# Performance work log

Measured on AMD Instinct MI355X. Metric: run time of the kernel, lower is better.

## Reference

```python
import jax, jax.numpy as jnp
import numpy as np

B, T, C = 1, 2048, 2048
H, KH, HD = 16, 4, 128  # n_head, n_kv_head, head_dim
ROPE_BASE = 10000.0


def setup_inputs() -> dict:
    key = jax.random.key(0)
    ks = jax.random.split(key, 5)
    s = 0.02
    return {
        "x": jax.random.normal(ks[0], (B, T, C), jnp.float32),
        "Wq": jax.random.normal(ks[1], (C, H * HD), jnp.float32) * s,
        "Wk": jax.random.normal(ks[2], (C, KH * HD), jnp.float32) * s,
        "Wv": jax.random.normal(ks[3], (C, KH * HD), jnp.float32) * s,
        "Wo": jax.random.normal(ks[4], (H * HD, C), jnp.float32) * s,
        "position_ids": jnp.arange(T, dtype=jnp.int32),
    }


def _rotate_half(a):
    h = a.shape[-1] // 2
    return jnp.concatenate([-a[..., h:], a[..., :h]], axis=-1)


def reference(x, Wq, Wk, Wv, Wo, position_ids):
    b, t, c = x.shape
    n_rep = H // KH
    # projections -> [B, heads, T, HD]
    q = (x @ Wq).reshape(b, t, H, HD).transpose(0, 2, 1, 3)
    k = (x @ Wk).reshape(b, t, KH, HD).transpose(0, 2, 1, 3)
    v = (x @ Wv).reshape(b, t, KH, HD).transpose(0, 2, 1, 3)
    # rotary embedding cache [T, HD]
    inv_freq = 1.0 / (ROPE_BASE ** (jnp.arange(0, HD, 2, dtype=jnp.float32) / HD))
    pos = jnp.arange(t, dtype=jnp.float32)
    freqs = pos[:, None] * inv_freq[None, :]
    emb = jnp.concatenate([freqs, freqs], axis=-1)
    cos = jnp.cos(emb)[position_ids][None, None]  # [1,1,T,HD]
    sin = jnp.sin(emb)[position_ids][None, None]
    q = q * cos + _rotate_half(q) * sin
    k = k * cos + _rotate_half(k) * sin
    # GQA: group query heads instead of materializing repeated K/V
    qg = q.reshape(b, KH, n_rep, t, HD)
    scale = jnp.float32(1.0 / np.sqrt(HD))
    scores = jnp.einsum('bgrtd,bgsd->bgrts', qg, k) * scale
    causal = jnp.tril(jnp.ones((t, t), dtype=bool))
    scores = jnp.where(causal, scores, jnp.float32(-1e30))
    p = jax.nn.softmax(scores, axis=-1)
    y = jnp.einsum('bgrts,bgsd->bgrtd', p, v)
    y = y.reshape(b, H, t, HD).transpose(0, 2, 1, 3).reshape(b, t, H * HD)
    return y @ Wo
```

## Files before the change

kernel.cpp:

```cpp
#include <hip/hip_runtime.h>

typedef unsigned short u16;
using bf16x8 = __attribute__((ext_vector_type(8))) short;
using f32x4  = __attribute__((ext_vector_type(4))) float;

#define GLD16(g, l)                                                            \
  __builtin_amdgcn_global_load_lds(                                            \
      (const __attribute__((address_space(1))) void*)(g),                      \
      (__attribute__((address_space(3))) void*)(l), 16, 0, 0)

__device__ __forceinline__ u16 f2b(float x) {
  union { float f; unsigned u; } v; v.f = x;
  unsigned r = v.u + 0x7FFF + ((v.u >> 16) & 1);
  return (u16)(r >> 16);
}

__global__ void cast_bf16_kernel(const float* __restrict__ in,
                                 u16* __restrict__ out, int n4) {
  int i = blockIdx.x * blockDim.x + threadIdx.x;
  int stride = gridDim.x * blockDim.x;
  for (; i < n4; i += stride) {
    float4 v = ((const float4*)in)[i];
    ushort4 o;
    o.x = f2b(v.x); o.y = f2b(v.y); o.z = f2b(v.z); o.w = f2b(v.w);
    ((ushort4*)out)[i] = o;
  }
}

__global__ void transpose_w_kernel(const float* __restrict__ src,
                                   u16* __restrict__ dst, int K, int N) {
  __shared__ float tile[32][33];
  int n0 = blockIdx.x * 32, k0 = blockIdx.y * 32;
  int tx = threadIdx.x, ty = threadIdx.y;
#pragma unroll
  for (int r = 0; r < 4; r++)
    tile[ty + r * 8][tx] = src[(size_t)(k0 + ty + r * 8) * N + n0 + tx];
  __syncthreads();
#pragma unroll
  for (int r = 0; r < 4; r++)
    dst[(size_t)(n0 + ty + r * 8) * K + k0 + tx] = f2b(tile[tx][ty + r * 8]);
}

__global__ void transpose_v_kernel(const u16* __restrict__ src,
                                   u16* __restrict__ dst) {
  __shared__ u16 tile[32][33];
  int h = blockIdx.z;
  int t0 = blockIdx.x * 32, d0 = blockIdx.y * 32;
  const u16* s = src + (size_t)h * 2048 * 128;
  u16* d = dst + (size_t)h * 128 * 2048;
  int tx = threadIdx.x, ty = threadIdx.y;
#pragma unroll
  for (int r = 0; r < 4; r++)
    tile[ty + r * 8][tx] = s[(size_t)(t0 + ty + r * 8) * 128 + d0 + tx];
  __syncthreads();
#pragma unroll
  for (int r = 0; r < 4; r++)
    d[(size_t)(d0 + ty + r * 8) * 2048 + t0 + tx] = tile[tx][ty + r * 8];
}

__global__ __launch_bounds__(256, 2)
void gemm_bt_128(const u16* __restrict__ A, const u16* __restrict__ Bt,
                 float* __restrict__ C, int M, int N, int K) {
  __shared__ u16 As[128 * 32];
  __shared__ u16 Bs[128 * 32];
  const int tid = threadIdx.x;
  const int lane = tid & 63;
  const int w = tid >> 6;
  const int wr = w >> 1, wc = w & 1;
  const int m0 = blockIdx.y * 128, n0 = blockIdx.x * 128;

  f32x4 acc[4][4] = {};

  const int srow = tid >> 2, skg = tid & 3;
  const u16* Ag0 = A + (size_t)(m0 + srow) * K + skg * 8;
  const u16* Ag1 = A + (size_t)(m0 + 64 + srow) * K + skg * 8;
  const u16* Bg0 = Bt + (size_t)(n0 + srow) * K + skg * 8;
  const u16* Bg1 = Bt + (size_t)(n0 + 64 + srow) * K + skg * 8;
  u16* Al0 = As + tid * 8;
  u16* Al1 = As + (256 + tid) * 8;
  u16* Bl0 = Bs + tid * 8;
  u16* Bl1 = Bs + (256 + tid) * 8;

  const int frow = lane & 15, fk = (lane >> 4) * 8;

  for (int k0 = 0; k0 < K; k0 += 32) {
    GLD16(Ag0 + k0, Al0);
    GLD16(Ag1 + k0, Al1);
    GLD16(Bg0 + k0, Bl0);
    GLD16(Bg1 + k0, Bl1);
    __syncthreads();
    bf16x8 av[4], bv[4];
#pragma unroll
    for (int m = 0; m < 4; m++)
      av[m] = *(const bf16x8*)(As + (wr * 64 + m * 16 + frow) * 32 + fk);
#pragma unroll
    for (int n = 0; n < 4; n++)
      bv[n] = *(const bf16x8*)(Bs + (wc * 64 + n * 16 + frow) * 32 + fk);
#pragma unroll
    for (int m = 0; m < 4; m++)
#pragma unroll
      for (int n = 0; n < 4; n++)
        acc[m][n] =
            __builtin_amdgcn_mfma_f32_16x16x32_bf16(av[m], bv[n], acc[m][n], 0, 0, 0);
    __syncthreads();
  }

  const int crow = (lane >> 4) * 4, ccol = lane & 15;
#pragma unroll
  for (int m = 0; m < 4; m++)
#pragma unroll
    for (int n = 0; n < 4; n++)
#pragma unroll
      for (int r = 0; r < 4; r++)
        C[(size_t)(m0 + wr * 64 + m * 16 + crow + r) * N +
          (n0 + wc * 64 + n * 16 + ccol)] = acc[m][n][r];
}

__global__ void rope_kernel(const float* __restrict__ QKV,
                            const int* __restrict__ pos, u16* __restrict__ Qb,
                            u16* __restrict__ Kb, u16* __restrict__ Vb) {
  const int t = blockIdx.x, tid = threadIdx.x;
  const float p = (float)pos[t];
  const float* row = QKV + (size_t)t * 3072;
  const float qscale = 0.08838834764831845f;
  const float c0 = -0.015625f * 13.287712379549449f;
#pragma unroll
  for (int i = 0; i < 4; i++) {
    int idx = tid + i * 256;
    int head = idx >> 6, d = idx & 63;
    float inv = exp2f((float)d * c0);
    float ang = p * inv;
    float s = sinf(ang), c = cosf(ang);
    float a0 = row[head * 128 + d], a1 = row[head * 128 + d + 64];
    Qb[((size_t)head * 2048 + t) * 128 + d] = f2b((a0 * c - a1 * s) * qscale);
    Qb[((size_t)head * 2048 + t) * 128 + d + 64] = f2b((a1 * c + a0 * s) * qscale);
  }
  {
    int head = tid >> 6, d = tid & 63;
    float inv = exp2f((float)d * c0);
    float ang = p * inv;
    float s = sinf(ang), c = cosf(ang);
    float a0 = row[2048 + head * 128 + d], a1 = row[2048 + head * 128 + d + 64];
    Kb[((size_t)head * 2048 + t) * 128 + d] = f2b(a0 * c - a1 * s);
    Kb[((size_t)head * 2048 + t) * 128 + d + 64] = f2b(a1 * c + a0 * s);
  }
#pragma unroll
  for (int i = 0; i < 2; i++) {
    int e = tid + i * 256;
    int kh = e >> 7, d = e & 127;
    Vb[((size_t)kh * 2048 + t) * 128 + d] = f2b(row[2560 + e]);
  }
}

__global__ __launch_bounds__(256, 2)
void attn_kernel(const u16* __restrict__ Qb, const u16* __restrict__ Kb,
                 const u16* __restrict__ Vtb, u16* __restrict__ Y) {
  __shared__ u16 Ks[2][64 * 128];
  __shared__ u16 Vs[2][128 * 64];
  __shared__ u16 Ps[4][16 * 64];
  const int tid = threadIdx.x, lane = tid & 63, w = tid >> 6;
  const int h = blockIdx.y, g = h >> 2;
  const int frow = lane & 15, fgrp = lane >> 4;
  const int t0 = blockIdx.x;
  const int t1 = 31 - t0;
  const int n0p = t0 + 1;

  const u16* Kg = Kb + (size_t)g * 2048 * 128;
  const u16* Vg = Vtb + (size_t)g * 128 * 2048;

#define STAGE(j0v, B)                                                          \
  {                                                                            \
    _Pragma("unroll")                                                          \
    for (int i = 0; i < 4; i++) {                                              \
      int p = tid + i * 256;                                                   \
      int kr = p >> 4, kc = (p & 15) ^ (kr & 7);                               \
      GLD16(Kg + (size_t)((j0v) + kr) * 128 + kc * 8, &Ks[B][p * 8]);          \
      int vr = p >> 3, vc = (p & 7) ^ (vr & 7);                                \
      GLD16(Vg + (size_t)vr * 2048 + (j0v) + vc * 8, &Vs[B][p * 8]);           \
    }                                                                          \
  }

  int qw = t0 * 64 + w * 16;
  bf16x8 qf[4];
  {
    const u16* Qrow = Qb + ((size_t)h * 2048 + (qw + frow)) * 128 + fgrp * 8;
#pragma unroll
    for (int kf = 0; kf < 4; kf++) qf[kf] = *(const bf16x8*)(Qrow + kf * 32);
  }

  f32x4 o[8] = {};
  float mrow[4], lrow[4];
#pragma unroll
  for (int r = 0; r < 4; r++) { mrow[r] = -1e30f; lrow[r] = 0.f; }

  STAGE(0, 0);
  __syncthreads();

  for (int it = 0; it < 33; ++it) {
    const int buf = it & 1;
    if (it + 1 < 33) {
      const int itn = it + 1;
      const int jn = (itn < n0p) ? itn : itn - n0p;
      STAGE(jn * 64, buf ^ 1);
    }
    if (it == n0p) {
#pragma unroll
      for (int r = 0; r < 4; r++) {
        float inv = 1.0f / lrow[r];
        int t = qw + fgrp * 4 + r;
#pragma unroll
        for (int db = 0; db < 8; db++)
          Y[(size_t)t * 2048 + h * 128 + db * 16 + frow] = f2b(o[db][r] * inv);
      }
#pragma unroll
      for (int db = 0; db < 8; db++)
#pragma unroll
        for (int r = 0; r < 4; r++) o[db][r] = 0.f;
#pragma unroll
      for (int r = 0; r < 4; r++) { mrow[r] = -1e30f; lrow[r] = 0.f; }
      qw = t1 * 64 + w * 16;
      const u16* Qrow = Qb + ((size_t)h * 2048 + (qw + frow)) * 128 + fgrp * 8;
#pragma unroll
      for (int kf = 0; kf < 4; kf++) qf[kf] = *(const bf16x8*)(Qrow + kf * 32);
    }
    const bool diag = (it == t0) || (it == 32);

    f32x4 sc[4] = {};
#pragma unroll
    for (int c = 0; c < 4; c++)
#pragma unroll
      for (int kf = 0; kf < 4; kf++) {
        int row = c * 16 + frow;
        bf16x8 kv = *(const bf16x8*)(
            &Ks[buf][row * 128 + ((kf * 4 + fgrp) ^ (row & 7)) * 8]);
        sc[c] = __builtin_amdgcn_mfma_f32_16x16x32_bf16(qf[kf], kv, sc[c], 0, 0, 0);
      }
    if (diag) {
#pragma unroll
      for (int c = 0; c < 4; c++) {
        int j = c * 16 + frow;
#pragma unroll
        for (int r = 0; r < 4; r++)
          if (j > (w * 16 + fgrp * 4 + r)) sc[c][r] = -1e30f;
      }
    }
    float pm[4];
#pragma unroll
    for (int r = 0; r < 4; r++)
      pm[r] = fmaxf(fmaxf(sc[0][r], sc[1][r]), fmaxf(sc[2][r], sc[3][r]));
#pragma unroll
    for (int off = 1; off < 16; off <<= 1)
#pragma unroll
      for (int r = 0; r < 4; r++) pm[r] = fmaxf(pm[r], __shfl_xor(pm[r], off, 64));
    bool nd = false;
#pragma unroll
    for (int r = 0; r < 4; r++) nd = nd || (pm[r] > mrow[r] + 8.f);
    if (__any(nd)) {
#pragma unroll
      for (int r = 0; r < 4; r++) {
        float mn = fmaxf(mrow[r], pm[r]);
        float alpha = __expf(mrow[r] - mn);
        mrow[r] = mn;
        lrow[r] *= alpha;
#pragma unroll
        for (int db = 0; db < 8; db++) o[db][r] *= alpha;
      }
    }
    float rs[4];
#pragma unroll
    for (int r = 0; r < 4; r++) {
      float s = 0.f;
#pragma unroll
      for (int c = 0; c < 4; c++) { sc[c][r] = __expf(sc[c][r] - mrow[r]); s += sc[c][r]; }
      rs[r] = s;
    }
#pragma unroll
    for (int off = 1; off < 16; off <<= 1)
#pragma unroll
      for (int r = 0; r < 4; r++) rs[r] += __shfl_xor(rs[r], off, 64);
#pragma unroll
    for (int r = 0; r < 4; r++) lrow[r] += rs[r];
    u16* Pw = Ps[w];
#pragma unroll
    for (int c = 0; c < 4; c++)
#pragma unroll
      for (int r = 0; r < 4; r++) {
        int row = fgrp * 4 + r, col = c * 16 + frow;
        Pw[row * 64 + (((col >> 3) ^ row) & 7) * 8 + (col & 7)] = f2b(sc[c][r]);
      }
    asm volatile("s_waitcnt lgkmcnt(0)" ::: "memory");
    bf16x8 pf[2];
#pragma unroll
    for (int ks = 0; ks < 2; ks++)
      pf[ks] = *(const bf16x8*)(
          &Pw[frow * 64 + ((ks * 4 + fgrp) ^ (frow & 7)) * 8]);
#pragma unroll
    for (int db = 0; db < 8; db++)
#pragma unroll
      for (int ks = 0; ks < 2; ks++) {
        int row = db * 16 + frow;
        bf16x8 vf = *(const bf16x8*)(
            &Vs[buf][row * 64 + ((ks * 4 + fgrp) ^ (row & 7)) * 8]);
        o[db] = __builtin_amdgcn_mfma_f32_16x16x32_bf16(pf[ks], vf, o[db], 0, 0, 0);
      }
    __syncthreads();
  }
#pragma unroll
  for (int r = 0; r < 4; r++) {
    float inv = 1.0f / lrow[r];
    int t = qw + fgrp * 4 + r;
#pragma unroll
    for (int db = 0; db < 8; db++)
      Y[(size_t)t * 2048 + h * 128 + db * 16 + frow] = f2b(o[db][r] * inv);
  }
#undef STAGE
}

extern "C" void kernel_launch(void* const* d_in, const int* in_sizes, int n_in,
                              void* d_out, int out_size, void* d_ws,
                              size_t ws_size, hipStream_t stream) {
  const float* x  = (const float*)d_in[0];
  const float* Wq = (const float*)d_in[1];
  const float* Wk = (const float*)d_in[2];
  const float* Wv = (const float*)d_in[3];
  const float* Wo = (const float*)d_in[4];
  const int* pos  = (const int*)d_in[5];
  float* out = (float*)d_out;
  char* ws = (char*)d_ws;

  u16* xb      = (u16*)(ws + 0);
  u16* Wqkv_bt = (u16*)(ws + 8388608);
  u16* Wo_bt   = (u16*)(ws + 20971520);
  float* QKV   = (float*)(ws + 29360128);
  u16* Yb      = (u16*)(ws + 29360128);
  u16* Qb      = (u16*)(ws + 54525952);
  u16* Kb      = (u16*)(ws + 62914560);
  u16* Vb      = (u16*)(ws + 65011712);
  u16* Vtb     = (u16*)(ws + 67108864);

  cast_bf16_kernel<<<1024, 256, 0, stream>>>(x, xb, 2048 * 2048 / 4);
  transpose_w_kernel<<<dim3(64, 64), dim3(32, 8), 0, stream>>>(Wq, Wqkv_bt, 2048, 2048);
  transpose_w_kernel<<<dim3(16, 64), dim3(32, 8), 0, stream>>>(Wk, Wqkv_bt + (size_t)2048 * 2048, 2048, 512);
  transpose_w_kernel<<<dim3(16, 64), dim3(32, 8), 0, stream>>>(Wv, Wqkv_bt + (size_t)2560 * 2048, 2048, 512);
  transpose_w_kernel<<<dim3(64, 64), dim3(32, 8), 0, stream>>>(Wo, Wo_bt, 2048, 2048);

  gemm_bt_128<<<dim3(3072 / 128, 2048 / 128), 256, 0, stream>>>(xb, Wqkv_bt, QKV, 2048, 3072, 2048);

  rope_kernel<<<2048, 256, 0, stream>>>(QKV, pos, Qb, Kb, Vb);
  transpose_v_kernel<<<dim3(64, 4, 4), dim3(32, 8), 0, stream>>>(Vb, Vtb);

  attn_kernel<<<dim3(16, 16), 256, 0, stream>>>(Qb, Kb, Vtb, Yb);

  gemm_bt_128<<<dim3(2048 / 128, 2048 / 128), 256, 0, stream>>>(Yb, Wo_bt, out, 2048, 2048, 2048);
}
```

Before: 271.0 us.

## Add 4-stage LDS ring buffer prefetch to bf16 GEMM main loop

```diff
diff --git a/kernel.cpp b/kernel.cpp
--- a/kernel.cpp
+++ b/kernel.cpp
@@ -61,8 +61,8 @@
 __global__ __launch_bounds__(256, 2)
 void gemm_bt_128(const u16* __restrict__ A, const u16* __restrict__ Bt,
                  float* __restrict__ C, int M, int N, int K) {
-  __shared__ u16 As[128 * 32];
-  __shared__ u16 Bs[128 * 32];
+  __shared__ u16 As[4][128 * 32];
+  __shared__ u16 Bs[4][128 * 32];
   const int tid = threadIdx.x;
   const int lane = tid & 63;
   const int w = tid >> 6;
@@ -76,34 +76,54 @@
   const u16* Ag1 = A + (size_t)(m0 + 64 + srow) * K + skg * 8;
   const u16* Bg0 = Bt + (size_t)(n0 + srow) * K + skg * 8;
   const u16* Bg1 = Bt + (size_t)(n0 + 64 + srow) * K + skg * 8;
-  u16* Al0 = As + tid * 8;
-  u16* Al1 = As + (256 + tid) * 8;
-  u16* Bl0 = Bs + tid * 8;
-  u16* Bl1 = Bs + (256 + tid) * 8;
+
+  const int l0 = tid * 8, l1 = (256 + tid) * 8;
+  u16 *pa0 = As[0], *pa1 = As[1], *pa2 = As[2], *pa3 = As[3];
+  u16 *pb0 = Bs[0], *pb1 = Bs[1], *pb2 = Bs[2], *pb3 = Bs[3];
+
+#define GSTAGE(k0v, pa, pb)                                                    \
+  {                                                                            \
+    GLD16(Ag0 + (k0v), (pa) + l0);                                             \
+    GLD16(Ag1 + (k0v), (pa) + l1);                                             \
+    GLD16(Bg0 + (k0v), (pb) + l0);                                             \
+    GLD16(Bg1 + (k0v), (pb) + l1);                                             \
+  }
+
+  GSTAGE(0, pa0, pb0);
+  GSTAGE(32, pa1, pb1);
 
   const int frow = lane & 15, fk = (lane >> 4) * 8;
-
-  for (int k0 = 0; k0 < K; k0 += 32) {
-    GLD16(Ag0 + k0, Al0);
-    GLD16(Ag1 + k0, Al1);
-    GLD16(Bg0 + k0, Bl0);
-    GLD16(Bg1 + k0, Bl1);
-    __syncthreads();
+  const int nk = K >> 5;
+
+  for (int i = 0; i < nk; ++i) {
+    if (i + 2 < nk) {
+      GSTAGE((i + 2) * 32, pa2, pb2);
+      asm volatile("s_waitcnt vmcnt(8)" ::: "memory");
+    } else if (i + 1 < nk) {
+      asm volatile("s_waitcnt vmcnt(4)" ::: "memory");
+    } else {
+      asm volatile("s_waitcnt vmcnt(0)" ::: "memory");
+    }
+    __builtin_amdgcn_s_barrier();
+    __builtin_amdgcn_sched_barrier(0);
     bf16x8 av[4], bv[4];
 #pragma unroll
     for (int m = 0; m < 4; m++)
-      av[m] = *(const bf16x8*)(As + (wr * 64 + m * 16 + frow) * 32 + fk);
+      av[m] = *(const bf16x8*)(pa0 + (wr * 64 + m * 16 + frow) * 32 + fk);
 #pragma unroll
     for (int n = 0; n < 4; n++)
-      bv[n] = *(const bf16x8*)(Bs + (wc * 64 + n * 16 + frow) * 32 + fk);
+      bv[n] = *(const bf16x8*)(pb0 + (wc * 64 + n * 16 + frow) * 32 + fk);
 #pragma unroll
     for (int m = 0; m < 4; m++)
 #pragma unroll
       for (int n = 0; n < 4; n++)
         acc[m][n] =
             __builtin_amdgcn_mfma_f32_16x16x32_bf16(av[m], bv[n], acc[m][n], 0, 0, 0);
-    __syncthreads();
-  }
+    u16* t;
+    t = pa0; pa0 = pa1; pa1 = pa2; pa2 = pa3; pa3 = t;
+    t = pb0; pb0 = pb1; pb1 = pb2; pb2 = pb3; pb3 = t;
+  }
+#undef GSTAGE
 
   const int crow = (lane >> 4) * 4, ccol = lane & 15;
 #pragma unroll
```

Result: faster. 263.8 us (-2.7%).
